# Kernel optimization log

Measured on AMD Instinct MI355X. Metric: run time of the kernel, lower is better.

Reference implementation:

```python
import jax, jax.numpy as jnp
import numpy as np

N_NODES = 100000
N_EDGES = 1600000
NFEATS, NHIDS, NOUT = 128, 128, 64


def _gcn_conv(x, W, b, src, dst, n_nodes):
    # PyG GCNConv: linear transform, then symmetric-normalized aggregation
    # over A + I (self-loops added), then bias.
    h = x @ W                                        # [N, out]
    loop = jnp.arange(n_nodes, dtype=src.dtype)
    s = jnp.concatenate([src, loop])                 # [E + N]
    d = jnp.concatenate([dst, loop])                 # [E + N]
    deg = jax.ops.segment_sum(jnp.ones_like(d, dtype=h.dtype), d,
                              num_segments=n_nodes)  # degree of A + I
    dinv = jnp.where(deg > 0, jax.lax.rsqrt(deg), 0.0)
    norm = dinv[s] * dinv[d]                         # [E + N]
    msg = h[s] * norm[:, None]                       # gather + scale
    out = jax.ops.segment_sum(msg, d, num_segments=n_nodes)  # scatter-add
    return out + b


def setup_inputs() -> dict:
    key = jax.random.key(0)
    k1, k2, k3, k4 = jax.random.split(key, 4)
    edge_index = jax.random.randint(k1, (2, N_EDGES), 0, N_NODES, dtype=jnp.int64)
    x = jax.random.normal(k2, (N_NODES, NFEATS), dtype=jnp.float32)
    W1 = jax.random.normal(k3, (NFEATS, NHIDS), dtype=jnp.float32) / np.sqrt(NFEATS)
    b1 = jnp.zeros((NHIDS,), dtype=jnp.float32)
    W2 = jax.random.normal(k4, (NHIDS, NOUT), dtype=jnp.float32) / np.sqrt(NHIDS)
    b2 = jnp.zeros((NOUT,), dtype=jnp.float32)
    return {"edge_index": edge_index, "x": x, "W1": W1, "b1": b1,
            "W2": W2, "b2": b2}


def reference(edge_index, x, W1, b1, W2, b2):
    src, dst = edge_index[0], edge_index[1]
    n = x.shape[0]
    h = jax.nn.relu(_gcn_conv(x, W1, b1, src, dst, n))
    # dropout(p=0.5, train=False) is the identity in eval mode
    out = _gcn_conv(h, W2, b2, src, dst, n)
    return out
```

## Files before the change

kernel.cpp:

```cpp
#include <hip/hip_runtime.h>
#include <cstdint>
#include <cstddef>

#define NFEATS 128
#define NHIDS  128
#define NOUT   64
#define SB     256
#define CHUNK  4096

using bf16x8 = __attribute__((ext_vector_type(8))) short;
using f32x4  = __attribute__((ext_vector_type(4))) float;

__device__ inline unsigned short f2bf(float f) {
    union { float f; unsigned int u; } v; v.f = f;
    unsigned int r = (v.u + 0x7FFFu + ((v.u >> 16) & 1u)) >> 16;
    return (unsigned short)r;
}
__device__ inline float bflo(unsigned int u) { return __uint_as_float(u << 16); }
__device__ inline float bfhi(unsigned int u) { return __uint_as_float(u & 0xFFFF0000u); }

__global__ void detect_kernel(const void* p, int* flag, long long n_nodes) {
    const long long* q = (const long long*)p;
    long long v = q[threadIdx.x];
    int bad = (v < 0 || v >= n_nodes) ? 1 : 0;
    unsigned long long m = __ballot(bad);
    if (threadIdx.x == 0) *flag = (m != 0ULL) ? 1 : 0;
}

__global__ void hist_kernel(const void* __restrict__ edges, const int* __restrict__ flag,
                            int* __restrict__ histT, int ne, int nch, int nbkt) {
    __shared__ int h[1024];
    int c = blockIdx.x, t = threadIdx.x;
    for (int i = t; i < nbkt; i += 512) h[i] = 0;
    __syncthreads();
    int beg = c * CHUNK, end = min(ne, beg + CHUNK);
    bool is32 = (*flag != 0);
    for (int i = beg + t; i < end; i += 512) {
        int d = is32 ? ((const int*)edges)[ne + i]
                     : (int)((const long long*)edges)[ne + i];
        atomicAdd(&h[d >> 8], 1);
    }
    __syncthreads();
    for (int i = t; i < nbkt; i += 512)
        histT[i * nch + c] = h[i];
}

__global__ void scan_block(const int* __restrict__ v, int* __restrict__ incl,
                           int* __restrict__ partial, int n) {
    __shared__ int sh[256];
    int t = threadIdx.x;
    int i = blockIdx.x * 256 + t;
    sh[t] = (i < n) ? v[i] : 0;
    __syncthreads();
    for (int off = 1; off < 256; off <<= 1) {
        int add = (t >= off) ? sh[t - off] : 0;
        __syncthreads();
        sh[t] += add;
        __syncthreads();
    }
    if (i < n) incl[i] = sh[t];
    if (t == 255) partial[blockIdx.x] = sh[255];
}

__global__ void scan_partials(int* partial, int nb) {
    __shared__ int sh[512];
    __shared__ int carry;
    int t = threadIdx.x;
    if (t == 0) carry = 0;
    __syncthreads();
    for (int base = 0; base < nb; base += 512) {
        int idx = base + t;
        sh[t] = (idx < nb) ? partial[idx] : 0;
        __syncthreads();
        for (int off = 1; off < 512; off <<= 1) {
            int add = (t >= off) ? sh[t - off] : 0;
            __syncthreads();
            sh[t] += add;
            __syncthreads();
        }
        int excl = carry + ((t == 0) ? 0 : sh[t - 1]);
        if (idx < nb) partial[idx] = excl;
        __syncthreads();
        if (t == 0) carry += sh[511];
        __syncthreads();
    }
}

__global__ void finalize_scan(const int* __restrict__ incl, const int* __restrict__ v,
                              const int* __restrict__ partial,
                              int* __restrict__ excl, int m) {
    int i = blockIdx.x * blockDim.x + threadIdx.x;
    if (i < m) excl[i] = partial[i >> 8] + incl[i] - v[i];
}

__global__ void scatter_chunks(const void* __restrict__ edges, const int* __restrict__ flag,
                               const int* __restrict__ chunk_base,
                               unsigned int* __restrict__ ebuf,
                               int ne, int nch, int nbkt) {
    __shared__ int cur[1024];
    int c = blockIdx.x, t = threadIdx.x;
    for (int i = t; i < nbkt; i += 512) cur[i] = chunk_base[i * nch + c];
    __syncthreads();
    int beg = c * CHUNK, end = min(ne, beg + CHUNK);
    bool is32 = (*flag != 0);
    for (int i = beg + t; i < end; i += 512) {
        int s, d;
        if (is32) {
            s = ((const int*)edges)[i];
            d = ((const int*)edges)[ne + i];
        } else {
            s = (int)((const long long*)edges)[i];
            d = (int)((const long long*)edges)[ne + i];
        }
        int pos = atomicAdd(&cur[d >> 8], 1);
        ebuf[pos] = ((unsigned int)s << 8) | (unsigned int)(d & (SB - 1));
    }
}

__global__ void bucket_finalize(const unsigned int* __restrict__ ebuf,
                                const int* __restrict__ chunk_base,
                                int* __restrict__ row_ptr, float* __restrict__ dinv,
                                int* __restrict__ csr_src,
                                int n, int e, int nch, int nbkt) {
    __shared__ int deg[SB];
    __shared__ int incl[SB];
    __shared__ int cur[SB];
    int b = blockIdx.x, t = threadIdx.x;
    int node0 = b * SB;
    int nn = min(SB, n - node0);
    int base = chunk_base[b * nch];
    int bend = (b == nbkt - 1) ? e : chunk_base[(b + 1) * nch];

    deg[t] = 0;
    __syncthreads();
    for (int i = base + t; i < bend; i += SB)
        atomicAdd(&deg[ebuf[i] & (SB - 1)], 1);
    __syncthreads();

    incl[t] = deg[t];
    __syncthreads();
    for (int off = 1; off < SB; off <<= 1) {
        int add = (t >= off) ? incl[t - off] : 0;
        __syncthreads();
        incl[t] += add;
        __syncthreads();
    }
    int lrow = base + incl[t] - deg[t];
    cur[t] = lrow;
    if (t < nn) {
        row_ptr[node0 + t] = lrow;
        dinv[node0 + t]    = rsqrtf((float)(deg[t] + 1));
    }
    if (b == nbkt - 1 && t == 0) row_ptr[n] = e;
    __syncthreads();

    for (int i = base + t; i < bend; i += SB) {
        unsigned int r = ebuf[i];
        int pos = atomicAdd(&cur[r & (SB - 1)], 1);
        csr_src[pos] = (int)(r >> 8);
    }
}

__global__ void wt_bf16(const float* __restrict__ W, unsigned short* __restrict__ Wt,
                        int K, int NC) {
    int i = blockIdx.x * blockDim.x + threadIdx.x;
    if (i < K * NC) {
        int k = i / NC, n = i % NC;
        Wt[n * K + k] = f2bf(W[i]);
    }
}

template <int NC, bool F32IN>
__launch_bounds__(256)
__global__ void gemm_mfma(const void* __restrict__ Xin,
                          const unsigned short* __restrict__ Wt,
                          const float* __restrict__ dinv,
                          unsigned short* __restrict__ hs, int nrows) {
    constexpr int K  = 128;
    constexpr int KP = 136;
    __shared__ __align__(16) unsigned short Xl[64 * KP];
    __shared__ __align__(16) unsigned short Wl[NC * KP];

    const int tid  = threadIdx.x;
    const int row0 = blockIdx.x * 64;

    for (int i = tid; i < 64 * (K / 4); i += 256) {
        int r  = i >> 5;
        int c4 = i & 31;
        int gr = row0 + r;
        ushort4 v = make_ushort4(0, 0, 0, 0);
        if (gr < nrows) {
            if (F32IN) {
                float4 f = ((const float4*)((const float*)Xin + (size_t)gr * K))[c4];
                v.x = f2bf(f.x); v.y = f2bf(f.y); v.z = f2bf(f.z); v.w = f2bf(f.w);
            } else {
                v = ((const ushort4*)((const unsigned short*)Xin + (size_t)gr * K))[c4];
            }
        }
        *(ushort4*)(Xl + r * KP + c4 * 4) = v;
    }
    for (int i = tid; i < NC * (K / 4); i += 256) {
        int r  = i >> 5;
        int c4 = i & 31;
        ushort4 v = ((const ushort4*)(Wt + (size_t)r * K))[c4];
        *(ushort4*)(Wl + r * KP + c4 * 4) = v;
    }
    __syncthreads();

    const int wv   = tid >> 6;
    const int lane = tid & 63;
    const int m    = lane & 15;
    const int q    = lane >> 4;

    bf16x8 af[4];
#pragma unroll
    for (int kt = 0; kt < 4; ++kt)
        af[kt] = *(const bf16x8*)(Xl + (wv * 16 + m) * KP + kt * 32 + q * 8);

    const int rbase = row0 + wv * 16 + q * 4;
    float dv[4];
#pragma unroll
    for (int i = 0; i < 4; ++i)
        dv[i] = (rbase + i < nrows) ? dinv[rbase + i] : 0.f;

#pragma unroll
    for (int nt = 0; nt < NC / 16; ++nt) {
        f32x4 acc = {0.f, 0.f, 0.f, 0.f};
#pragma unroll
        for (int kt = 0; kt < 4; ++kt) {
            bf16x8 bfr = *(const bf16x8*)(Wl + (nt * 16 + m) * KP + kt * 32 + q * 8);
            acc = __builtin_amdgcn_mfma_f32_16x16x32_bf16(af[kt], bfr, acc, 0, 0, 0);
        }
#pragma unroll
        for (int i = 0; i < 4; ++i) {
            int g = rbase + i;
            if (g < nrows)
                hs[(size_t)g * NC + nt * 16 + m] = f2bf(acc[i] * dv[i]);
        }
    }
}

template <int F, bool RELU, bool OUTBF>
__launch_bounds__(256)
__global__ void aggregate_bf16(const int* __restrict__ row_ptr,
                               const int* __restrict__ csr_src,
                               const uint4* __restrict__ hsu,
                               const float* __restrict__ dinv,
                               const float* __restrict__ b,
                               void* __restrict__ out, int n) {
    constexpr int TPN = F / 8;
    constexpr int NPB = 256 / TPN;
    int node = blockIdx.x * NPB + threadIdx.x / TPN;
    int t    = threadIdx.x % TPN;
    if (node >= n) return;

    uint4 u = hsu[(size_t)node * TPN + t];
    float a[8];
    a[0] = bflo(u.x); a[1] = bfhi(u.x); a[2] = bflo(u.y); a[3] = bfhi(u.y);
    a[4] = bflo(u.z); a[5] = bfhi(u.z); a[6] = bflo(u.w); a[7] = bfhi(u.w);

    int beg = row_ptr[node], end = row_ptr[node + 1];
    for (int e = beg; e < end; e += 8) {
        int rem = end - e;
        int s[8];
#pragma unroll
        for (int j = 0; j < 8; ++j)
            s[j] = csr_src[e + (j < rem ? j : 0)];
        uint4 v[8];
#pragma unroll
        for (int j = 0; j < 8; ++j)
            v[j] = hsu[(size_t)s[j] * TPN + t];
#pragma unroll
        for (int j = 0; j < 8; ++j) {
            if (j < rem) {
                a[0] += bflo(v[j].x); a[1] += bfhi(v[j].x);
                a[2] += bflo(v[j].y); a[3] += bfhi(v[j].y);
                a[4] += bflo(v[j].z); a[5] += bfhi(v[j].z);
                a[6] += bflo(v[j].w); a[7] += bfhi(v[j].w);
            }
        }
    }

    float dvn = dinv[node];
    float4 b0 = ((const float4*)b)[2 * t];
    float4 b1 = ((const float4*)b)[2 * t + 1];
    float o[8];
    o[0] = a[0] * dvn + b0.x; o[1] = a[1] * dvn + b0.y;
    o[2] = a[2] * dvn + b0.z; o[3] = a[3] * dvn + b0.w;
    o[4] = a[4] * dvn + b1.x; o[5] = a[5] * dvn + b1.y;
    o[6] = a[6] * dvn + b1.z; o[7] = a[7] * dvn + b1.w;
    if (RELU) {
#pragma unroll
        for (int j = 0; j < 8; ++j) o[j] = fmaxf(o[j], 0.f);
    }
    if (OUTBF) {
        uint4 ov;
        ov.x = (unsigned int)f2bf(o[0]) | ((unsigned int)f2bf(o[1]) << 16);
        ov.y = (unsigned int)f2bf(o[2]) | ((unsigned int)f2bf(o[3]) << 16);
        ov.z = (unsigned int)f2bf(o[4]) | ((unsigned int)f2bf(o[5]) << 16);
        ov.w = (unsigned int)f2bf(o[6]) | ((unsigned int)f2bf(o[7]) << 16);
        ((uint4*)out)[(size_t)node * TPN + t] = ov;
    } else {
        float4* op = (float4*)out + (size_t)node * (F / 4) + 2 * t;
        op[0] = make_float4(o[0], o[1], o[2], o[3]);
        op[1] = make_float4(o[4], o[5], o[6], o[7]);
    }
}

extern "C" void kernel_launch(void* const* d_in, const int* in_sizes, int n_in,
                              void* d_out, int out_size, void* d_ws, size_t ws_size,
                              hipStream_t stream) {
    const void*  edge = d_in[0];
    const float* x    = (const float*)d_in[1];
    const float* W1   = (const float*)d_in[2];
    const float* b1   = (const float*)d_in[3];
    const float* W2   = (const float*)d_in[4];
    const float* b2   = (const float*)d_in[5];
    float* out = (float*)d_out;

    const int E    = in_sizes[0] / 2;
    const int N    = in_sizes[1] / NFEATS;
    const int NBKT = (N + SB - 1) / SB;
    const int NCH  = (E + CHUNK - 1) / CHUNK;
    const int M    = NBKT * NCH;

    char* w = (char*)d_ws;
    auto carve = [&](size_t bytes) { void* p = w; w += (bytes + 255) & ~(size_t)255; return p; };
    int*            flag       = (int*)           carve(256);
    int*            histT      = (int*)           carve(sizeof(int) * (size_t)M);
    int*            incl       = (int*)           carve(sizeof(int) * (size_t)M);
    int*            partial    = (int*)           carve(sizeof(int) * 4096);
    int*            chunk_base = (int*)           carve(sizeof(int) * (size_t)M);
    int*            row_ptr    = (int*)           carve(sizeof(int) * ((size_t)N + 1));
    float*          dinv       = (float*)         carve(sizeof(float) * (size_t)N);
    unsigned int*   ebuf       = (unsigned int*)  carve(sizeof(int) * (size_t)E);
    int*            csr_src    = (int*)           carve(sizeof(int) * (size_t)E);
    unsigned short* Wt1        = (unsigned short*)carve(2 * (size_t)NFEATS * NHIDS);
    unsigned short* Wt2        = (unsigned short*)carve(2 * (size_t)NHIDS * NOUT);
    unsigned short* hs1        = (unsigned short*)carve(2 * (size_t)N * NHIDS);
    unsigned short* h1         = (unsigned short*)carve(2 * (size_t)N * NHIDS);
    unsigned short* hs2        = (unsigned short*)carve(2 * (size_t)N * NOUT);

    const int B   = 256;
    const int nbS = (M + 255) / 256;

    detect_kernel<<<1, 64, 0, stream>>>(edge, flag, (long long)N);

    hist_kernel<<<NCH, 512, 0, stream>>>(edge, flag, histT, E, NCH, NBKT);
    scan_block<<<nbS, 256, 0, stream>>>(histT, incl, partial, M);
    scan_partials<<<1, 512, 0, stream>>>(partial, nbS);
    finalize_scan<<<nbS, 256, 0, stream>>>(incl, histT, partial, chunk_base, M);
    scatter_chunks<<<NCH, 512, 0, stream>>>(edge, flag, chunk_base, ebuf, E, NCH, NBKT);
    bucket_finalize<<<NBKT, SB, 0, stream>>>(ebuf, chunk_base, row_ptr, dinv, csr_src,
                                             N, E, NCH, NBKT);

    wt_bf16<<<(NFEATS * NHIDS + B - 1) / B, B, 0, stream>>>(W1, Wt1, NFEATS, NHIDS);
    wt_bf16<<<(NHIDS * NOUT + B - 1) / B, B, 0, stream>>>(W2, Wt2, NHIDS, NOUT);

    gemm_mfma<NHIDS, true><<<(N + 63) / 64, B, 0, stream>>>(x, Wt1, dinv, hs1, N);
    {
        constexpr int NPB = 256 / (NHIDS / 8);
        aggregate_bf16<NHIDS, true, true><<<(N + NPB - 1) / NPB, B, 0, stream>>>(
            row_ptr, csr_src, (const uint4*)hs1, dinv, b1, h1, N);
    }

    gemm_mfma<NOUT, false><<<(N + 63) / 64, B, 0, stream>>>(h1, Wt2, dinv, hs2, N);
    {
        constexpr int NPB = 256 / (NOUT / 8);
        aggregate_bf16<NOUT, false, false><<<(N + NPB - 1) / NPB, B, 0, stream>>>(
            row_ptr, csr_src, (const uint4*)hs2, dinv, b2, out, N);
    }
}
```

Measured before the change: 293.3 us.

## Pre-pack weights in MFMA fragment layout and double GEMM rows per block

```diff
diff --git a/kernel.cpp b/kernel.cpp
--- a/kernel.cpp
+++ b/kernel.cpp
@@ -161,30 +161,32 @@
     }
 }
 
-__global__ void wt_bf16(const float* __restrict__ W, unsigned short* __restrict__ Wt,
-                        int K, int NC) {
+__global__ void w_pack(const float* __restrict__ W1, unsigned short* __restrict__ Wf1,
+                       const float* __restrict__ W2, unsigned short* __restrict__ Wf2) {
     int i = blockIdx.x * blockDim.x + threadIdx.x;
-    if (i < K * NC) {
-        int k = i / NC, n = i % NC;
-        Wt[n * K + k] = f2bf(W[i]);
+    if (i < 128 * 128) {
+        int k = i >> 7, n = i & 127;
+        Wf1[(((k >> 3) * 128) + n) * 8 + (k & 7)] = f2bf(W1[i]);
+    }
+    if (i < 128 * 64) {
+        int k = i >> 6, n = i & 63;
+        Wf2[(((k >> 3) * 64) + n) * 8 + (k & 7)] = f2bf(W2[i]);
     }
 }
 
 template <int NC, bool F32IN>
 __launch_bounds__(256)
 __global__ void gemm_mfma(const void* __restrict__ Xin,
-                          const unsigned short* __restrict__ Wt,
+                          const unsigned short* __restrict__ Wf,
                           const float* __restrict__ dinv,
                           unsigned short* __restrict__ hs, int nrows) {
-    constexpr int K  = 128;
-    constexpr int KP = 136;
-    __shared__ __align__(16) unsigned short Xl[64 * KP];
-    __shared__ __align__(16) unsigned short Wl[NC * KP];
+    constexpr int K = 128;
+    __shared__ __align__(16) unsigned short Xl[16 * 128 * 8];
 
     const int tid  = threadIdx.x;
-    const int row0 = blockIdx.x * 64;
-
-    for (int i = tid; i < 64 * (K / 4); i += 256) {
+    const int row0 = blockIdx.x * 128;
+
+    for (int i = tid; i < 128 * 32; i += 256) {
         int r  = i >> 5;
         int c4 = i & 31;
         int gr = row0 + r;
@@ -197,13 +199,10 @@
                 v = ((const ushort4*)((const unsigned short*)Xin + (size_t)gr * K))[c4];
             }
         }
-        *(ushort4*)(Xl + r * KP + c4 * 4) = v;
-    }
-    for (int i = tid; i < NC * (K / 4); i += 256) {
-        int r  = i >> 5;
-        int c4 = i & 31;
-        ushort4 v = ((const ushort4*)(Wt + (size_t)r * K))[c4];
-        *(ushort4*)(Wl + r * KP + c4 * 4) = v;
+        int k   = c4 * 4;
+        int grp = k >> 3;
+        int j0  = k & 7;
+        *(ushort4*)(Xl + ((size_t)grp * 128 + r) * 8 + j0) = v;
     }
     __syncthreads();
 
@@ -212,30 +211,41 @@
     const int m    = lane & 15;
     const int q    = lane >> 4;
 
-    bf16x8 af[4];
-#pragma unroll
-    for (int kt = 0; kt < 4; ++kt)
-        af[kt] = *(const bf16x8*)(Xl + (wv * 16 + m) * KP + kt * 32 + q * 8);
-
-    const int rbase = row0 + wv * 16 + q * 4;
-    float dv[4];
-#pragma unroll
-    for (int i = 0; i < 4; ++i)
-        dv[i] = (rbase + i < nrows) ? dinv[rbase + i] : 0.f;
+    bf16x8 af[2][4];
+#pragma unroll
+    for (int h = 0; h < 2; ++h)
+#pragma unroll
+        for (int kt = 0; kt < 4; ++kt)
+            af[h][kt] = *(const bf16x8*)(Xl + (((kt * 4 + q) * 128) + h * 64 + wv * 16 + m) * 8);
+
+    int   rbase[2];
+    float dv[2][4];
+#pragma unroll
+    for (int h = 0; h < 2; ++h) {
+        rbase[h] = row0 + h * 64 + wv * 16 + q * 4;
+#pragma unroll
+        for (int i = 0; i < 4; ++i)
+            dv[h][i] = (rbase[h] + i < nrows) ? dinv[rbase[h] + i] : 0.f;
+    }
 
 #pragma unroll
     for (int nt = 0; nt < NC / 16; ++nt) {
-        f32x4 acc = {0.f, 0.f, 0.f, 0.f};
-#pragma unroll
-        for (int kt = 0; kt < 4; ++kt) {
-            bf16x8 bfr = *(const bf16x8*)(Wl + (nt * 16 + m) * KP + kt * 32 + q * 8);
-            acc = __builtin_amdgcn_mfma_f32_16x16x32_bf16(af[kt], bfr, acc, 0, 0, 0);
-        }
-#pragma unroll
-        for (int i = 0; i < 4; ++i) {
-            int g = rbase + i;
-            if (g < nrows)
-                hs[(size_t)g * NC + nt * 16 + m] = f2bf(acc[i] * dv[i]);
+        bf16x8 bfr[4];
+#pragma unroll
+        for (int kt = 0; kt < 4; ++kt)
+            bfr[kt] = *(const bf16x8*)(Wf + (((size_t)(kt * 4 + q) * NC) + nt * 16 + m) * 8);
+#pragma unroll
+        for (int h = 0; h < 2; ++h) {
+            f32x4 acc = {0.f, 0.f, 0.f, 0.f};
+#pragma unroll
+            for (int kt = 0; kt < 4; ++kt)
+                acc = __builtin_amdgcn_mfma_f32_16x16x32_bf16(af[h][kt], bfr[kt], acc, 0, 0, 0);
+#pragma unroll
+            for (int i = 0; i < 4; ++i) {
+                int g = rbase[h] + i;
+                if (g < nrows)
+                    hs[(size_t)g * NC + nt * 16 + m] = f2bf(acc[i] * dv[h][i]);
+            }
         }
     }
 }
@@ -335,8 +345,8 @@
     float*          dinv       = (float*)         carve(sizeof(float) * (size_t)N);
     unsigned int*   ebuf       = (unsigned int*)  carve(sizeof(int) * (size_t)E);
     int*            csr_src    = (int*)           carve(sizeof(int) * (size_t)E);
-    unsigned short* Wt1        = (unsigned short*)carve(2 * (size_t)NFEATS * NHIDS);
-    unsigned short* Wt2        = (unsigned short*)carve(2 * (size_t)NHIDS * NOUT);
+    unsigned short* Wf1        = (unsigned short*)carve(2 * (size_t)NFEATS * NHIDS);
+    unsigned short* Wf2        = (unsigned short*)carve(2 * (size_t)NHIDS * NOUT);
     unsigned short* hs1        = (unsigned short*)carve(2 * (size_t)N * NHIDS);
     unsigned short* h1         = (unsigned short*)carve(2 * (size_t)N * NHIDS);
     unsigned short* hs2        = (unsigned short*)carve(2 * (size_t)N * NOUT);
@@ -354,17 +364,16 @@
     bucket_finalize<<<NBKT, SB, 0, stream>>>(ebuf, chunk_base, row_ptr, dinv, csr_src,
                                              N, E, NCH, NBKT);
 
-    wt_bf16<<<(NFEATS * NHIDS + B - 1) / B, B, 0, stream>>>(W1, Wt1, NFEATS, NHIDS);
-    wt_bf16<<<(NHIDS * NOUT + B - 1) / B, B, 0, stream>>>(W2, Wt2, NHIDS, NOUT);
-
-    gemm_mfma<NHIDS, true><<<(N + 63) / 64, B, 0, stream>>>(x, Wt1, dinv, hs1, N);
+    w_pack<<<(128 * 128 + B - 1) / B, B, 0, stream>>>(W1, Wf1, W2, Wf2);
+
+    gemm_mfma<NHIDS, true><<<(N + 127) / 128, B, 0, stream>>>(x, Wf1, dinv, hs1, N);
     {
         constexpr int NPB = 256 / (NHIDS / 8);
         aggregate_bf16<NHIDS, true, true><<<(N + NPB - 1) / NPB, B, 0, stream>>>(
             row_ptr, csr_src, (const uint4*)hs1, dinv, b1, h1, N);
     }
 
-    gemm_mfma<NOUT, false><<<(N + 63) / 64, B, 0, stream>>>(h1, Wt2, dinv, hs2, N);
+    gemm_mfma<NOUT, false><<<(N + 127) / 128, B, 0, stream>>>(h1, Wf2, dinv, hs2, N);
     {
         constexpr int NPB = 256 / (NOUT / 8);
         aggregate_bf16<NOUT, false, false><<<(N + NPB - 1) / NPB, B, 0, stream>>>(
```

Result: faster. 277.0 us (-5.6%).
